# Kernel optimization log

Measured on AMD Instinct MI355X. Metric: run time of the kernel, lower is better.

Reference implementation:

```python
import jax, jax.numpy as jnp
import numpy as np

N0, N1, N2 = 100000, 300000, 150000
P = 2
DIM = 64


def spmm(rows, cols, vals, dense, n_rows):
    # sparse[n_rows, n_cols] @ dense[n_cols, d] via gather + segment_sum
    return jax.ops.segment_sum(vals[:, None] * dense[cols], rows, num_segments=n_rows)


def powcat(X, p):
    # torch.cat([X**1, ..., X**p], dim=1)
    return jnp.concatenate([X ** n for n in range(1, p + 1)], axis=1)


def setup_inputs() -> dict:
    key = jax.random.key(0)
    ks = iter(jax.random.split(key, 64))

    def randn(shape, scale=1.0):
        return jax.random.normal(next(ks), shape, dtype=jnp.float32) * scale

    def sparse(nr, nc, nnz):
        r = jax.random.randint(next(ks), (nnz,), 0, nr, dtype=jnp.int32)
        c = jax.random.randint(next(ks), (nnz,), 0, nc, dtype=jnp.int32)
        v = randn((nnz,), 0.1)
        return r, c, v

    inp = {}
    inp["X0"] = randn((N0, DIM))
    inp["X1"] = randn((N1, DIM))
    inp["X2"] = randn((N2, DIM))
    for name, nr, nc, nnz in [
        ("L0", N0, N0, 1000000),
        ("L1", N1, N1, 2400000),
        ("L2", N2, N2, 1200000),
        ("D1invB1", N0, N1, 600000),
        ("D2B1TD1inv", N1, N0, 600000),
        ("B2TD2inv", N2, N1, 450000),
        ("B2D3", N1, N2, 450000),
    ]:
        r, c, v = sparse(nr, nc, nnz)
        inp[name + "_rows"], inp[name + "_cols"], inp[name + "_vals"] = r, c, v
    wscale = 1.0 / np.sqrt(DIM * P)
    for name in ["n2n", "n2e", "e2e", "e2n", "e2t", "t2e", "t2t"]:
        inp["W_" + name] = randn((DIM * P, DIM), wscale)
        inp["b_" + name] = randn((DIM,), wscale)
    return inp


def reference(X0, X1, X2,
              L0_rows, L0_cols, L0_vals,
              L1_rows, L1_cols, L1_vals,
              L2_rows, L2_cols, L2_vals,
              D1invB1_rows, D1invB1_cols, D1invB1_vals,
              D2B1TD1inv_rows, D2B1TD1inv_cols, D2B1TD1inv_vals,
              B2TD2inv_rows, B2TD2inv_cols, B2TD2inv_vals,
              B2D3_rows, B2D3_cols, B2D3_vals,
              W_n2n, b_n2n, W_n2e, b_n2e, W_e2e, b_e2e, W_e2n, b_e2n,
              W_e2t, b_e2t, W_t2e, b_t2e, W_t2t, b_t2t):
    X0c = powcat(X0, P)  # [N0, 2*d]
    X1c = powcat(X1, P)  # [N1, 2*d]
    X2c = powcat(X2, P)  # [N2, 2*d]

    n2n = spmm(L0_rows, L0_cols, L0_vals, X0c @ W_n2n + b_n2n, N0)
    n2e = spmm(D2B1TD1inv_rows, D2B1TD1inv_cols, D2B1TD1inv_vals, X0c @ W_n2e + b_n2e, N1)
    e2n = spmm(D1invB1_rows, D1invB1_cols, D1invB1_vals, X1c @ W_e2n + b_e2n, N0)
    e2e = spmm(L1_rows, L1_cols, L1_vals, X1c @ W_e2e + b_e2e, N1)
    e2t = spmm(B2TD2inv_rows, B2TD2inv_cols, B2TD2inv_vals, X1c @ W_e2t + b_e2t, N2)
    t2t = spmm(L2_rows, L2_cols, L2_vals, X2c @ W_t2t + b_t2t, N2)
    t2e = spmm(B2D3_rows, B2D3_cols, B2D3_vals, X2c @ W_t2e + b_t2e, N1)

    Y0 = 0.5 * jax.nn.relu(n2n + e2n)
    Y1 = (1.0 / 3.0) * jax.nn.relu(e2e + n2e + t2e)
    Y2 = 0.5 * jax.nn.relu(t2t + e2t)
    return (Y0, Y1, Y2)
```

## Files before the change

### kernel.cpp

```cpp
#include <hip/hip_runtime.h>
#include <hip/hip_bf16.h>


#define RPB 128
#define COL_MASK 0x7FFFFu
#define LROW_SH 19
#define DID_SH 26
#define MAXNB 4352
#define MAXNG 544
#define GRID_BIN 256
#define SPMM_GRID 2048

#define SORT_PH     16384
#define SORT_LOG    14
#define SORT_MAXBIN 2048
#define SORT_CAP    (SORT_PH + SORT_MAXBIN)
#define MAXPH 8

typedef __attribute__((ext_vector_type(8))) short short8;
typedef __attribute__((ext_vector_type(4))) float f32x4;

__device__ __forceinline__ int   ntld_i(const int* p)   { return __builtin_nontemporal_load(p); }
__device__ __forceinline__ float ntld_f(const float* p) { return __builtin_nontemporal_load(p); }
__device__ __forceinline__ float4 ntld_f4(const float* p) {
    const unsigned long long* q = (const unsigned long long*)p;
    unsigned long long a = __builtin_nontemporal_load(q);
    unsigned long long b = __builtin_nontemporal_load(q + 1);
    float4 v;
    v.x = __uint_as_float((unsigned)a);
    v.y = __uint_as_float((unsigned)(a >> 32));
    v.z = __uint_as_float((unsigned)b);
    v.w = __uint_as_float((unsigned)(b >> 32));
    return v;
}
__device__ __forceinline__ void ntst_f4(float* p, float4 v) {
    unsigned long long a = (unsigned long long)__float_as_uint(v.x)
                         | ((unsigned long long)__float_as_uint(v.y) << 32);
    unsigned long long b = (unsigned long long)__float_as_uint(v.z)
                         | ((unsigned long long)__float_as_uint(v.w) << 32);
    unsigned long long* q = (unsigned long long*)p;
    __builtin_nontemporal_store(a, q);
    __builtin_nontemporal_store(b, q + 1);
}

__device__ __forceinline__ unsigned short f2bf(float f) {
    unsigned u = __float_as_uint(f);
    unsigned r = u + 0x7FFFu + ((u >> 16) & 1u);
    return (unsigned short)(r >> 16);
}

__device__ __forceinline__ void split8(float4 a0, float4 a1, short8& hi, short8& lo) {
    float v[8] = {a0.x, a0.y, a0.z, a0.w, a1.x, a1.y, a1.z, a1.w};
    #pragma unroll
    for (int e = 0; e < 8; ++e) {
        unsigned short h = f2bf(v[e]);
        float hf = __uint_as_float((unsigned)h << 16);
        hi[e] = (short)h;
        lo[e] = (short)f2bf(v[e] - hf);
    }
}

struct WAll { const float* w[7]; };

__global__ __launch_bounds__(256) void winit(WAll wa, unsigned short* __restrict__ frags)
{
    const int s = blockIdx.x;
    const float* __restrict__ W = wa.w[s];
    unsigned short* __restrict__ out = frags + (size_t)s * 16384;
    for (int slot = threadIdx.x; slot < 1024; slot += 256) {
        const int l  = slot & 63;
        const int nf = (slot >> 6) & 3;
        const int kk = slot >> 8;
        const int col = nf * 16 + (l & 15);
        const int kb  = kk * 32 + 8 * (l >> 4);
        short8 vh, vl;
        #pragma unroll
        for (int e = 0; e < 8; ++e) {
            float w = W[(size_t)(kb + e) * 64 + col];
            unsigned short h = f2bf(w);
            float hf = __uint_as_float((unsigned)h << 16);
            vh[e] = (short)h;
            vl[e] = (short)f2bf(w - hf);
        }
        *(short8*)(out + ((size_t)((kk * 4 + nf) * 2 + 0) * 64 + l) * 8) = vh;
        *(short8*)(out + ((size_t)((kk * 4 + nf) * 2 + 1) * 64 + l) * 8) = vl;
    }
}

__device__ __forceinline__ void mfma_set(
    const short8 Ah[4], const short8 Al[4],
    const unsigned short* __restrict__ F, const float* __restrict__ bias,
    unsigned short* __restrict__ D, int nrows, int row0w, int l)
{
    const int lg = l >> 4, lr = l & 15;
    const short8* __restrict__ Fv = (const short8*)F;
    f32x4 acc[4];
    #pragma unroll
    for (int nf = 0; nf < 4; ++nf) {
        float b = bias[nf * 16 + lr];
        f32x4 bi = {b, b, b, b};
        acc[nf] = bi;
    }
    #pragma unroll
    for (int kk = 0; kk < 4; ++kk) {
        #pragma unroll
        for (int nf = 0; nf < 4; ++nf) {
            short8 bh = Fv[((kk * 4 + nf) * 2 + 0) * 64 + l];
            short8 bl = Fv[((kk * 4 + nf) * 2 + 1) * 64 + l];
            acc[nf] = __builtin_amdgcn_mfma_f32_16x16x32_bf16(Ah[kk], bh, acc[nf], 0, 0, 0);
            acc[nf] = __builtin_amdgcn_mfma_f32_16x16x32_bf16(Al[kk], bh, acc[nf], 0, 0, 0);
            acc[nf] = __builtin_amdgcn_mfma_f32_16x16x32_bf16(Ah[kk], bl, acc[nf], 0, 0, 0);
        }
    }
    #pragma unroll
    for (int nf = 0; nf < 4; ++nf) {
        #pragma unroll
        for (int j = 0; j < 4; ++j) {
            int row = row0w + lg * 4 + j;
            if (row < nrows)
                D[(size_t)row * 64 + nf * 16 + lr] = f2bf(acc[nf][j]);
        }
    }
}

__global__ __launch_bounds__(256) void gemm_powcat_mfma(
    const float* __restrict__ X, int nrows, int nsets,
    const unsigned short* __restrict__ F0, const float* __restrict__ b0, unsigned short* __restrict__ D0,
    const unsigned short* __restrict__ F1, const float* __restrict__ b1, unsigned short* __restrict__ D1,
    const unsigned short* __restrict__ F2, const float* __restrict__ b2, unsigned short* __restrict__ D2)
{
    __shared__ float Xs[64][68];
    const int tid = threadIdx.x;
    const int row0 = blockIdx.x * 64;

    #pragma unroll
    for (int it = 0; it < 4; ++it) {
        int idx = tid + it * 256;
        int r = idx >> 4, c4 = idx & 15;
        float4 v = make_float4(0.f, 0.f, 0.f, 0.f);
        if (row0 + r < nrows)
            v = ntld_f4(X + (size_t)(row0 + r) * 64 + c4 * 4);
        *(float4*)&Xs[r][c4 * 4] = v;
    }
    __syncthreads();

    const int w = tid >> 6, l = tid & 63;
    const int lg = l >> 4, lr = l & 15;

    short8 Ah[4], Al[4];
    #pragma unroll
    for (int kk = 0; kk < 4; ++kk) {
        const float* p = &Xs[w * 16 + lr][(kk & 1) * 32 + 8 * lg];
        float4 a0 = *(const float4*)p;
        float4 a1 = *(const float4*)(p + 4);
        if (kk >= 2) {
            a0.x *= a0.x; a0.y *= a0.y; a0.z *= a0.z; a0.w *= a0.w;
            a1.x *= a1.x; a1.y *= a1.y; a1.z *= a1.z; a1.w *= a1.w;
        }
        split8(a0, a1, Ah[kk], Al[kk]);
    }

    const int row0w = row0 + w * 16;
    mfma_set(Ah, Al, F0, b0, D0, nrows, row0w, l);
    if (nsets > 1) mfma_set(Ah, Al, F1, b1, D1, nrows, row0w, l);
    if (nsets > 2) mfma_set(Ah, Al, F2, b2, D2, nrows, row0w, l);
}

struct Bin7 {
    const int *r0, *r1, *r2, *r3, *r4, *r5, *r6;
    const int *c0, *c1, *c2, *c3, *c4, *c5, *c6;
    const float *v0, *v1, *v2, *v3, *v4, *v5, *v6;
    int p1, p2, p3, p4, p5, p6, p7;
    int t0, t1, t2, t3, t4, t5, t6;
};

struct Ent { int r; int tb; unsigned cw; float v; };

template<bool FULL>
__device__ __forceinline__ Ent decode(const Bin7& B, int i) {
    Ent e;
    if (i < B.p1) {
        int li = i;
        e.r = ntld_i(B.r0 + li); e.tb = B.t0;
        if (FULL) { e.cw = (unsigned)ntld_i(B.c0 + li) | (0u << DID_SH); e.v = ntld_f(B.v0 + li); }
    } else if (i < B.p2) {
        int li = i - B.p1;
        e.r = ntld_i(B.r1 + li); e.tb = B.t1;
        if (FULL) { e.cw = (unsigned)ntld_i(B.c1 + li) | (1u << DID_SH); e.v = ntld_f(B.v1 + li); }
    } else if (i < B.p3) {
        int li = i - B.p2;
        e.r = ntld_i(B.r2 + li); e.tb = B.t2;
        if (FULL) { e.cw = (unsigned)ntld_i(B.c2 + li) | (2u << DID_SH); e.v = ntld_f(B.v2 + li); }
    } else if (i < B.p4) {
        int li = i - B.p3;
        e.r = ntld_i(B.r3 + li); e.tb = B.t3;
        if (FULL) { e.cw = (unsigned)ntld_i(B.c3 + li) | (3u << DID_SH); e.v = ntld_f(B.v3 + li); }
    } else if (i < B.p5) {
        int li = i - B.p4;
        e.r = ntld_i(B.r4 + li); e.tb = B.t4;
        if (FULL) { e.cw = (unsigned)ntld_i(B.c4 + li) | (4u << DID_SH); e.v = ntld_f(B.v4 + li); }
    } else if (i < B.p6) {
        int li = i - B.p5;
        e.r = ntld_i(B.r5 + li); e.tb = B.t5;
        if (FULL) { e.cw = (unsigned)ntld_i(B.c5 + li) | (5u << DID_SH); e.v = ntld_f(B.v5 + li); }
    } else {
        int li = i - B.p6;
        e.r = ntld_i(B.r6 + li); e.tb = B.t6;
        if (FULL) { e.cw = (unsigned)ntld_i(B.c6 + li) | (6u << DID_SH); e.v = ntld_f(B.v6 + li); }
    }
    return e;
}

__global__ __launch_bounds__(1024) void bhist_grp(
    Bin7 B, int* __restrict__ gcount, int NG, int chunk)
{
    __shared__ int h[MAXNG];
    for (int i = threadIdx.x; i < NG; i += 1024) h[i] = 0;
    __syncthreads();
    const int s = blockIdx.x * chunk;
    int e = s + chunk;  if (e > B.p7) e = B.p7;
    for (int i = s + threadIdx.x; i < e; i += 1024) {
        Ent en = decode<false>(B, i);
        atomicAdd(&h[(en.tb + (en.r >> 7)) >> 3], 1);
    }
    __syncthreads();
    for (int i = threadIdx.x; i < NG; i += 1024)
        if (h[i]) atomicAdd(&gcount[i], h[i]);
}

__global__ __launch_bounds__(1024) void scatter_grp(
    Bin7 B, int* __restrict__ gcur, uint2* __restrict__ payA,
    int NG, int chunk)
{
    __shared__ int lbase[MAXNG];
    __shared__ int lcur[MAXNG];
    for (int i = threadIdx.x; i < NG; i += 1024) lcur[i] = 0;
    __syncthreads();
    const int s = blockIdx.x * chunk;
    int e = s + chunk;  if (e > B.p7) e = B.p7;

    for (int i = s + threadIdx.x; i < e; i += 1024) {
        Ent en = decode<false>(B, i);
        atomicAdd(&lcur[(en.tb + (en.r >> 7)) >> 3], 1);
    }
    __syncthreads();
    for (int i = threadIdx.x; i < NG; i += 1024) {
        int c = lcur[i];
        lbase[i] = c ? atomicAdd(&gcur[i], c) : 0;
        lcur[i] = 0;
    }
    __syncthreads();
    for (int i = s + threadIdx.x; i < e; i += 1024) {
        Ent en = decode<true>(B, i);
        int b = en.tb + (en.r >> 7);
        int g = b >> 3;
        int pos = lbase[g] + atomicAdd(&lcur[g], 1);
        unsigned col = en.cw & COL_MASK;
        unsigned did = en.cw >> DID_SH;
        unsigned cwA = col | ((unsigned)(en.r & 127) << LROW_SH)
                     | ((unsigned)(b & 7) << 26) | (did << 29);
        payA[pos] = make_uint2(cwA, __float_as_uint(en.v));
    }
}

__global__ __launch_bounds__(1024) void sort_grp(
    const uint2* __restrict__ payA, const int* __restrict__ goff,
    const int* __restrict__ gcur, int* __restrict__ rowoff,
    int* __restrict__ bend, uint2* __restrict__ payB, int NBtot)
{
    __shared__ uint2 lpay[SORT_CAP];
    __shared__ int cnt[1024];
    __shared__ int off[1024];
    __shared__ int wsum[16];
    __shared__ int phstart[MAXPH + 1];
    __shared__ int s_nph, s_maxbin;

    const int g = blockIdx.x;
    const int tid = threadIdx.x;
    const int seg0 = goff[g], seg1 = gcur[g];
    const int n = seg1 - seg0;

    cnt[tid] = 0;
    if (tid == 0) s_maxbin = 0;
    __syncthreads();
    for (int i = seg0 + tid; i < seg1; i += 1024) {
        unsigned w = __builtin_nontemporal_load(&payA[i].x);
        atomicAdd(&cnt[(w >> 19) & 1023], 1);
    }
    __syncthreads();

    const int lane = tid & 63, wv = tid >> 6;
    const int tot = cnt[tid];
    atomicMax(&s_maxbin, tot);
    int x = tot;
    #pragma unroll
    for (int o = 1; o < 64; o <<= 1) {
        int y = __shfl_up(x, o);
        if (lane >= o) x += y;
    }
    if (lane == 63) wsum[wv] = x;
    __syncthreads();
    if (tid < 16) {
        int ss = wsum[tid];
        #pragma unroll
        for (int o = 1; o < 16; o <<= 1) {
            int y = __shfl_up(ss, o, 16);
            if (tid >= o) ss += y;
        }
        wsum[tid] = ss;
    }
    __syncthreads();
    const int excl = (x - tot) + ((wv == 0) ? 0 : wsum[wv - 1]);
    off[tid] = excl;
    rowoff[(size_t)g * 1024 + tid] = seg0 + excl;
    {
        int b = g * 8 + (tid >> 7);
        if (b < NBtot && (tid & 127) == 127) bend[b] = seg0 + excl + tot;
    }
    __syncthreads();
    cnt[tid] = excl;
    {
        int p = excl >> SORT_LOG;
        int pprev = (tid == 0) ? -1 : (off[tid - 1] >> SORT_LOG);
        for (int q = pprev + 1; q <= p && q <= MAXPH; ++q) phstart[q] = excl;
        if (tid == 1023) s_nph = p + 1;
    }
    __syncthreads();

    const int nph = s_nph;
    if (n <= 0) return;

    if (s_maxbin <= SORT_MAXBIN && nph <= MAXPH) {
        for (int ph = 0; ph < nph; ++ph) {
            const int ps = phstart[ph];
            const int pe = (ph + 1 < nph) ? phstart[ph + 1] : n;
            for (int i = seg0 + tid; i < seg1; i += 1024) {
                unsigned long long pv = __builtin_nontemporal_load(
                    (const unsigned long long*)(payA + i));
                unsigned w = (unsigned)pv;
                int bin = (w >> 19) & 1023;
                if ((off[bin] >> SORT_LOG) == ph) {
                    int pos = atomicAdd(&cnt[bin], 1);
                    lpay[pos - ps] = make_uint2(w, (unsigned)(pv >> 32));
                }
            }
            __syncthreads();
            for (int k = tid; k < pe - ps; k += 1024) {
                uint2 pv = lpay[k];
                unsigned cw = (pv.x & 0x03FFFFFFu) | ((pv.x >> 29) << 26);
                unsigned long long o2 = (unsigned long long)cw
                                      | ((unsigned long long)pv.y << 32);
                __builtin_nontemporal_store(o2,
                    (unsigned long long*)(payB + seg0 + ps + k));
            }
            __syncthreads();
        }
    } else {
        for (int i = seg0 + tid; i < seg1; i += 1024) {
            unsigned long long pv = __builtin_nontemporal_load(
                (const unsigned long long*)(payA + i));
            unsigned w = (unsigned)pv;
            int bin = (w >> 19) & 1023;
            int pos = seg0 + atomicAdd(&cnt[bin], 1);
            unsigned cw = (w & 0x03FFFFFFu) | ((w >> 29) << 26);
            payB[pos] = make_uint2(cw, (unsigned)(pv >> 32));
        }
    }
}

__global__ __launch_bounds__(1024) void scan_small(
    const int* __restrict__ in, int* __restrict__ boff,
    int* __restrict__ bcur, int n)
{
    __shared__ int wsum[16];
    __shared__ int carry;
    const int tid = threadIdx.x, lane = tid & 63, wv = tid >> 6;
    if (tid == 0) carry = 0;
    __syncthreads();
    for (int base = 0; base < n; base += 4096) {
        int i = base + tid * 4;
        int v0 = (i + 0 < n) ? in[i + 0] : 0;
        int v1 = (i + 1 < n) ? in[i + 1] : 0;
        int v2 = (i + 2 < n) ? in[i + 2] : 0;
        int v3 = (i + 3 < n) ? in[i + 3] : 0;
        int tsum = v0 + v1 + v2 + v3;
        int x = tsum;
        #pragma unroll
        for (int off = 1; off < 64; off <<= 1) {
            int y = __shfl_up(x, off);
            if (lane >= off) x += y;
        }
        if (lane == 63) wsum[wv] = x;
        int c0 = carry;
        __syncthreads();
        if (tid < 16) {
            int ss = wsum[tid];
            #pragma unroll
            for (int off = 1; off < 16; off <<= 1) {
                int y = __shfl_up(ss, off, 16);
                if (tid >= off) ss += y;
            }
            wsum[tid] = ss;
        }
        __syncthreads();
        int wpre = (wv == 0) ? 0 : wsum[wv - 1];
        int excl = c0 + wpre + (x - tsum);
        if (i + 0 < n) { boff[i + 0] = excl; bcur[i + 0] = excl; } excl += v0;
        if (i + 1 < n) { boff[i + 1] = excl; bcur[i + 1] = excl; } excl += v1;
        if (i + 2 < n) { boff[i + 2] = excl; bcur[i + 2] = excl; } excl += v2;
        if (i + 3 < n) { boff[i + 3] = excl; bcur[i + 3] = excl; }
        __syncthreads();
        if (tid == 0) carry = c0 + wsum[15];
        __syncthreads();
    }
}

__device__ __forceinline__ float mval(uint2 p, int didMask) {
    int did = (int)(p.x >> DID_SH) & 7;
    return ((didMask >> did) & 1) ? __uint_as_float(p.y) : 0.f;
}
__device__ __forceinline__ uint2 dgather(uint2 p, int l,
    const unsigned short* const* dptr)
{
    const uint2* Dg = reinterpret_cast<const uint2*>(dptr[(p.x >> DID_SH) & 7]);
    return Dg[(size_t)(p.x & COL_MASK) * 16 + l];
}
__device__ __forceinline__ void facc(float4& a, float v, uint2 d) {
    a.x = fmaf(v, __uint_as_float((d.x & 0xFFFFu) << 16), a.x);
    a.y = fmaf(v, __uint_as_float(d.x & 0xFFFF0000u), a.y);
    a.z = fmaf(v, __uint_as_float((d.y & 0xFFFFu) << 16), a.z);
    a.w = fmaf(v, __uint_as_float(d.y & 0xFFFF0000u), a.w);
}

__device__ __forceinline__ float4 row_accum(
    const uint2* __restrict__ payB, int js, int je,
    const unsigned short* const* dptr, int l, int didMask)
{
    float4 a = make_float4(0.f, 0.f, 0.f, 0.f);
    const int n = je - js;
    if (n <= 0) return a;
    const uint2* base = payB + js;
    uint2 p0 = base[0];
    uint2 p1 = base[(n > 1) ? 1 : 0];
    float v0 = mval(p0, didMask);
    float v1 = (n > 1) ? mval(p1, didMask) : 0.f;
    uint2 d0 = dgather(p0, l, dptr);
    uint2 d1 = dgather(p1, l, dptr);
    int i = 0;
    while (true) {
        int i2 = (i + 2 < n) ? i + 2 : n - 1;
        int i3 = (i + 3 < n) ? i + 3 : n - 1;
        uint2 q0 = base[i2];
        uint2 q1 = base[i3];
        float w0 = (i + 2 < n) ? mval(q0, didMask) : 0.f;
        float w1 = (i + 3 < n) ? mval(q1, didMask) : 0.f;
        uint2 e0 = dgather(q0, l, dptr);
        uint2 e1 = dgather(q1, l, dptr);
        facc(a, v0, d0);
        facc(a, v1, d1);
        i += 2;
        if (i >= n) break;
        v0 = w0; v1 = w1; d0 = e0; d1 = e1;
    }
    return a;
}

__global__ __launch_bounds__(256) void spmm_stream_all(
    const uint2* __restrict__ payB, const int* __restrict__ rowoff,
    const int* __restrict__ bend,
    const unsigned short* __restrict__ d0, const unsigned short* __restrict__ d1,
    const unsigned short* __restrict__ d2, const unsigned short* __restrict__ d3,
    const unsigned short* __restrict__ d4, const unsigned short* __restrict__ d5,
    const unsigned short* __restrict__ d6,
    float* __restrict__ out, int NB0, int NB01, int NBall,
    int N0, int N1, int N2)
{
    __shared__ const unsigned short* dptr[8];
    const int tid = threadIdx.x;
    if (tid < 8) {
        const unsigned short* tbl[8] = {d0, d1, d2, d3, d4, d5, d6, d0};
        dptr[tid] = tbl[tid];
    }
    __syncthreads();

    const int qw = tid >> 4, l = tid & 15;

    for (int t = blockIdx.x; t < NBall; t += gridDim.x) {
        int tb, nrows; float scale; float* oseg;
        if (t < NB0)       { tb = 0;    nrows = N0; oseg = out;                          scale = 0.5f; }
        else if (t < NB01) { tb = NB0;  nrows = N1; oseg = out + (size_t)N0 * 64;        scale = 1.0f / 3.0f; }
        else               { tb = NB01; nrows = N2; oseg = out + (size_t)(N0 + N1) * 64; scale = 0.5f; }
        const int row0 = (t - tb) * RPB;
        const int rbase = t * RPB;
        const int bendt = bend[t];

        #pragma unroll 1
        for (int rr = 0; rr < 8; ++rr) {
            const int lr = rr * 16 + qw;
            const int row = row0 + lr;
            const int js = rowoff[rbase + lr];
            const int je = (lr == 127) ? bendt : rowoff[rbase + lr + 1];
            float4 a = row_accum(payB, js, je, dptr, l, 0x7F);
            if (row < nrows) {
                float* o = oseg + (size_t)row * 64 + l * 4;
                a.x = fmaxf(a.x, 0.f) * scale;
                a.y = fmaxf(a.y, 0.f) * scale;
                a.z = fmaxf(a.z, 0.f) * scale;
                a.w = fmaxf(a.w, 0.f) * scale;
                ntst_f4(o, a);
            }
        }
    }
}

__global__ __launch_bounds__(256) void spmm_stream7(
    const uint2* __restrict__ payB, const int* __restrict__ rowoff,
    const int* __restrict__ bend,
    const unsigned short* __restrict__ d0, const unsigned short* __restrict__ d1,
    const unsigned short* __restrict__ d2, const unsigned short* __restrict__ d3,
    const unsigned short* __restrict__ d4, const unsigned short* __restrict__ d5,
    const unsigned short* __restrict__ d6,
    float* __restrict__ out, int tile0, int nrows,
    int firstWrite, int doRelu, float scale, int didMask)
{
    __shared__ const unsigned short* dptr[8];
    const int tid = threadIdx.x;
    if (tid < 8) {
        const unsigned short* tbl[8] = {d0, d1, d2, d3, d4, d5, d6, d0};
        dptr[tid] = tbl[tid];
    }
    __syncthreads();

    const int t = tile0 + blockIdx.x;
    const int qw = tid >> 4, l = tid & 15;
    const int row0 = blockIdx.x * RPB;
    const int rbase = t * RPB;
    const int bendt = bend[t];

    #pragma unroll 1
    for (int rr = 0; rr < 8; ++rr) {
        const int lr = rr * 16 + qw;
        const int row = row0 + lr;
        const int js = rowoff[rbase + lr];
        const int je = (lr == 127) ? bendt : rowoff[rbase + lr + 1];
        float4 a = row_accum(payB, js, je, dptr, l, didMask);

        if (row < nrows) {
            float* o = out + (size_t)row * 64 + l * 4;
            if (!firstWrite) {
                float4 cur = *reinterpret_cast<float4*>(o);
                a.x += cur.x; a.y += cur.y; a.z += cur.z; a.w += cur.w;
            }
            if (doRelu) {
                a.x = fmaxf(a.x, 0.f) * scale;
                a.y = fmaxf(a.y, 0.f) * scale;
                a.z = fmaxf(a.z, 0.f) * scale;
                a.w = fmaxf(a.w, 0.f) * scale;
            }
            ntst_f4(o, a);
        }
    }
}

extern "C" void kernel_launch(void* const* d_in, const int* in_sizes, int n_in,
                              void* d_out, int out_size, void* d_ws, size_t ws_size,
                              hipStream_t stream)
{
    const float* X0 = (const float*)d_in[0];
    const float* X1 = (const float*)d_in[1];
    const float* X2 = (const float*)d_in[2];
    const int N0 = in_sizes[0] / 64;
    const int N1 = in_sizes[1] / 64;
    const int N2 = in_sizes[2] / 64;

    auto Wp = [&](int i) { return (const float*)d_in[24 + 2 * i]; };
    auto bp = [&](int i) { return (const float*)d_in[25 + 2 * i]; };
    auto Sr = [&](int i) { return (const int*)d_in[3 + 3 * i]; };
    auto Sc = [&](int i) { return (const int*)d_in[4 + 3 * i]; };
    auto Sv = [&](int i) { return (const float*)d_in[5 + 3 * i]; };
    auto Sn = [&](int i) { return in_sizes[3 + 3 * i]; };

    const size_t offY1 = (size_t)N0 * 64;
    const size_t offY2 = (size_t)(N0 + N1) * 64;
    const float TH = 1.0f / 3.0f;

    const int NB0 = (N0 + RPB - 1) / RPB;
    const int NB1 = (N1 + RPB - 1) / RPB;
    const int NB2 = (N2 + RPB - 1) / RPB;

    float* out = (float*)d_out;
    auto align256 = [](size_t x) { return (x + 255) & ~(size_t)255; };

    const size_t FRAG_SET = 16384;
    const size_t fragB = align256(7 * FRAG_SET * sizeof(unsigned short));
    if (ws_size <= fragB) return;
    unsigned short* wfrags = (unsigned short*)d_ws;
    char* ws = (char*)d_ws + fragB;
    const size_t ws_avail = ws_size - fragB;
    auto wf = [&](int i) { return wfrags + (size_t)i * FRAG_SET; };

    WAll wa;
    for (int i = 0; i < 7; ++i) wa.w[i] = Wp(i);
    winit<<<7, 256, 0, stream>>>(wa, wfrags);

    const int NBall = NB0 + NB1 + NB2;
    const int NGall = (NBall + 7) / 8;
    const int nnzAll = Sn(0)+Sn(1)+Sn(2)+Sn(3)+Sn(4)+Sn(5)+Sn(6);
    const size_t payT1 = align256((size_t)nnzAll * sizeof(uint2));
    const size_t cntT1 = align256((size_t)(NBall + 8) * sizeof(int));
    const size_t rowT1 = align256((size_t)NGall * 1024 * sizeof(int));
    const size_t denseT1 = ((size_t)2*N0 + 3*N1 + 2*N2) * 64 * sizeof(unsigned short);
    const size_t regionT1 = denseT1 > payT1 ? denseT1 : payT1;
    const size_t needT1 = payT1 + 4 * cntT1 + rowT1 + regionT1;

    if (ws_avail >= needT1 && NBall <= MAXNB) {
        uint2* payB  = (uint2*)ws;
        int* goff    = (int*)(ws + payT1);
        int* gcur    = (int*)(ws + payT1 + 1 * cntT1);
        int* bend    = (int*)(ws + payT1 + 2 * cntT1);
        int* gcount  = (int*)(ws + payT1 + 3 * cntT1);
        int* rowoff  = (int*)(ws + payT1 + 4 * cntT1);
        char* region = ws + payT1 + 4 * cntT1 + rowT1;
        uint2* payA  = (uint2*)region;
        unsigned short* db = (unsigned short*)region;
        unsigned short* dn2n = db;
        unsigned short* de2n = dn2n + (size_t)N0 * 64;
        unsigned short* dn2e = de2n + (size_t)N1 * 64;
        unsigned short* de2e = dn2e + (size_t)N0 * 64;
        unsigned short* dt2e = de2e + (size_t)N1 * 64;
        unsigned short* de2t = dt2e + (size_t)N2 * 64;
        unsigned short* dt2t = de2t + (size_t)N1 * 64;

        Bin7 B;
        B.r0 = Sr(0); B.c0 = Sc(0); B.v0 = Sv(0);
        B.r1 = Sr(3); B.c1 = Sc(3); B.v1 = Sv(3);
        B.r2 = Sr(4); B.c2 = Sc(4); B.v2 = Sv(4);
        B.r3 = Sr(1); B.c3 = Sc(1); B.v3 = Sv(1);
        B.r4 = Sr(6); B.c4 = Sc(6); B.v4 = Sv(6);
        B.r5 = Sr(5); B.c5 = Sc(5); B.v5 = Sv(5);
        B.r6 = Sr(2); B.c6 = Sc(2); B.v6 = Sv(2);
        B.p1 = Sn(0);
        B.p2 = B.p1 + Sn(3);
        B.p3 = B.p2 + Sn(4);
        B.p4 = B.p3 + Sn(1);
        B.p5 = B.p4 + Sn(6);
        B.p6 = B.p5 + Sn(5);
        B.p7 = B.p6 + Sn(2);
        B.t0 = 0;   B.t1 = 0;
        B.t2 = NB0; B.t3 = NB0; B.t4 = NB0;
        B.t5 = NB0 + NB1; B.t6 = NB0 + NB1;

        const int chunk = (B.p7 + GRID_BIN - 1) / GRID_BIN;
        hipMemsetAsync(gcount, 0, (size_t)NGall * sizeof(int), stream);
        bhist_grp<<<GRID_BIN, 1024, 0, stream>>>(B, gcount, NGall, chunk);
        scan_small<<<1, 1024, 0, stream>>>(gcount, goff, gcur, NGall);
        scatter_grp<<<GRID_BIN, 1024, 0, stream>>>(B, gcur, payA, NGall, chunk);
        sort_grp<<<NGall, 1024, 0, stream>>>(payA, goff, gcur, rowoff, bend, payB, NBall);

        gemm_powcat_mfma<<<(N0 + 63) / 64, 256, 0, stream>>>(
            X0, N0, 2,
            wf(0), bp(0), dn2n,
            wf(1), bp(1), dn2e,
            wf(0), bp(0), dn2n);
        gemm_powcat_mfma<<<(N1 + 63) / 64, 256, 0, stream>>>(
            X1, N1, 3,
            wf(3), bp(3), de2n,
            wf(2), bp(2), de2e,
            wf(4), bp(4), de2t);
        gemm_powcat_mfma<<<(N2 + 63) / 64, 256, 0, stream>>>(
            X2, N2, 2,
            wf(5), bp(5), dt2e,
            wf(6), bp(6), dt2t,
            wf(5), bp(5), dt2e);

        const int grid = NBall < SPMM_GRID ? NBall : SPMM_GRID;
        spmm_stream_all<<<grid, 256, 0, stream>>>(payB, rowoff, bend,
            dn2n, de2n, dn2e, de2e, dt2e, de2t, dt2t,
            out, NB0, NB0 + NB1, NBall, N0, N1, N2);
        return;
    }

    const int NBtotA = NB0 + NB2;
    const int NBmax = NBtotA > NB1 ? NBtotA : NB1;
    const int NGmax = (NBmax + 7) / 8;
    const int nnzA = Sn(0) + Sn(3) + Sn(5) + Sn(2);
    const int nnzB = Sn(4) + Sn(6) + Sn(1);
    const int nnzMax = nnzA > nnzB ? nnzA : nnzB;

    const size_t payBsz = align256((size_t)nnzMax * sizeof(uint2));
    const size_t cntB = align256((size_t)(NBmax + 8) * sizeof(int));
    const size_t rowB = align256((size_t)NGmax * 1024 * sizeof(int));
    const size_t denseOff = payBsz + 4 * cntB + rowB;

    uint2* bpayB = (uint2*)ws;
    int* goff    = (int*)(ws + payBsz);
    int* gcur    = (int*)(ws + payBsz + 1 * cntB);
    int* bend    = (int*)(ws + payBsz + 2 * cntB);
    int* gcount  = (int*)(ws + payBsz + 3 * cntB);
    int* rowoff  = (int*)(ws + payBsz + 4 * cntB);
    unsigned short* dense = (unsigned short*)(ws + denseOff);
    uint2* payA  = (uint2*)dense;

    const size_t need_full = denseOff +
        ((size_t)N0 + N2 + N1) * 64 * sizeof(unsigned short);
    const bool fullB = (ws_avail >= need_full);

    {
        Bin7 B;
        B.r0 = Sr(0); B.c0 = Sc(0); B.v0 = Sv(0);
        B.r1 = Sr(3); B.c1 = Sc(3); B.v1 = Sv(3);
        B.r2 = Sr(5); B.c2 = Sc(5); B.v2 = Sv(5);
        B.r3 = Sr(2); B.c3 = Sc(2); B.v3 = Sv(2);
        B.r4 = B.r3; B.c4 = B.c3; B.v4 = B.v3;
        B.r5 = B.r3; B.c5 = B.c3; B.v5 = B.v3;
        B.r6 = B.r3; B.c6 = B.c3; B.v6 = B.v3;
        B.p1 = Sn(0);
        B.p2 = B.p1 + Sn(3);
        B.p3 = B.p2 + Sn(5);
        B.p4 = B.p3 + Sn(2);
        B.p5 = B.p4; B.p6 = B.p4; B.p7 = B.p4;
        B.t0 = 0; B.t1 = 0; B.t2 = NB0; B.t3 = NB0;
        B.t4 = NB0; B.t5 = NB0; B.t6 = NB0;

        const int NGA = (NBtotA + 7) / 8;
        const int chunk = (B.p7 + GRID_BIN - 1) / GRID_BIN;
        hipMemsetAsync(gcount, 0, (size_t)NGA * sizeof(int), stream);
        bhist_grp<<<GRID_BIN, 1024, 0, stream>>>(B, gcount, NGA, chunk);
        scan_small<<<1, 1024, 0, stream>>>(gcount, goff, gcur, NGA);
        scatter_grp<<<GRID_BIN, 1024, 0, stream>>>(B, gcur, payA, NGA, chunk);
        sort_grp<<<NGA, 1024, 0, stream>>>(payA, goff, gcur, rowoff, bend, bpayB, NBtotA);

        unsigned short* dn2n = dense;
        unsigned short* de2n = dense + (size_t)N0 * 64;
        gemm_powcat_mfma<<<(N0 + 63) / 64, 256, 0, stream>>>(
            X0, N0, 1, wf(0), bp(0), dn2n,
            wf(0), bp(0), dn2n, wf(0), bp(0), dn2n);
        gemm_powcat_mfma<<<(N1 + 63) / 64, 256, 0, stream>>>(
            X1, N1, 1, wf(3), bp(3), de2n,
            wf(3), bp(3), de2n, wf(3), bp(3), de2n);
        spmm_stream7<<<NB0, 256, 0, stream>>>(bpayB, rowoff, bend,
            dn2n, de2n, dn2n, dn2n, dn2n, dn2n, dn2n,
            out, 0, N0, 1, 1, 0.5f, 0x7F);

        unsigned short* de2t = dense;
        unsigned short* dt2t = dense + (size_t)N1 * 64;
        gemm_powcat_mfma<<<(N1 + 63) / 64, 256, 0, stream>>>(
            X1, N1, 1, wf(4), bp(4), de2t,
            wf(4), bp(4), de2t, wf(4), bp(4), de2t);
        gemm_powcat_mfma<<<(N2 + 63) / 64, 256, 0, stream>>>(
            X2, N2, 1, wf(6), bp(6), dt2t,
            wf(6), bp(6), dt2t, wf(6), bp(6), dt2t);
        spmm_stream7<<<NB2, 256, 0, stream>>>(bpayB, rowoff, bend,
            de2t, de2t, de2t, dt2t, de2t, de2t, de2t,
            out + offY2, NB0, N2, 1, 1, 0.5f, 0x7F);
    }

    {
        Bin7 B;
        B.r0 = Sr(4); B.c0 = Sc(4); B.v0 = Sv(4);
        B.r1 = Sr(6); B.c1 = Sc(6); B.v1 = Sv(6);
        B.r2 = Sr(1); B.c2 = Sc(1); B.v2 = Sv(1);
        B.r3 = B.r2; B.c3 = B.c2; B.v3 = B.v2;
        B.r4 = B.r2; B.c4 = B.c2; B.v4 = B.v2;
        B.r5 = B.r2; B.c5 = B.c2; B.v5 = B.v2;
        B.r6 = B.r2; B.c6 = B.c2; B.v6 = B.v2;
        B.p1 = Sn(4);
        B.p2 = B.p1 + Sn(6);
        B.p3 = B.p2 + Sn(1);
        B.p4 = B.p3; B.p5 = B.p3; B.p6 = B.p3; B.p7 = B.p3;
        B.t0 = 0; B.t1 = 0; B.t2 = 0; B.t3 = 0; B.t4 = 0; B.t5 = 0; B.t6 = 0;

        const int NGB = (NB1 + 7) / 8;
        const int chunk = (B.p7 + GRID_BIN - 1) / GRID_BIN;
        hipMemsetAsync(gcount, 0, (size_t)NGB * sizeof(int), stream);
        bhist_grp<<<GRID_BIN, 1024, 0, stream>>>(B, gcount, NGB, chunk);
        scan_small<<<1, 1024, 0, stream>>>(gcount, goff, gcur, NGB);
        scatter_grp<<<GRID_BIN, 1024, 0, stream>>>(B, gcur, payA, NGB, chunk);
        sort_grp<<<NGB, 1024, 0, stream>>>(payA, goff, gcur, rowoff, bend, bpayB, NB1);

        if (fullB) {
            unsigned short* dn2e = dense;
            unsigned short* dt2e = dense + (size_t)N0 * 64;
            unsigned short* de2e = dense + ((size_t)N0 + N2) * 64;
            gemm_powcat_mfma<<<(N0 + 63) / 64, 256, 0, stream>>>(
                X0, N0, 1, wf(1), bp(1), dn2e,
                wf(1), bp(1), dn2e, wf(1), bp(1), dn2e);
            gemm_powcat_mfma<<<(N2 + 63) / 64, 256, 0, stream>>>(
                X2, N2, 1, wf(5), bp(5), dt2e,
                wf(5), bp(5), dt2e, wf(5), bp(5), dt2e);
            gemm_powcat_mfma<<<(N1 + 63) / 64, 256, 0, stream>>>(
                X1, N1, 1, wf(2), bp(2), de2e,
                wf(2), bp(2), de2e, wf(2), bp(2), de2e);
            spmm_stream7<<<NB1, 256, 0, stream>>>(bpayB, rowoff, bend,
                dn2e, dt2e, de2e, dn2e, dn2e, dn2e, dn2e,
                out + offY1, 0, N1, 1, 1, TH, 0x7F);
        } else {
            unsigned short* dn2e = dense;
            unsigned short* dt2e = dense + (size_t)N0 * 64;
            gemm_powcat_mfma<<<(N0 + 63) / 64, 256, 0, stream>>>(
                X0, N0, 1, wf(1), bp(1), dn2e,
                wf(1), bp(1), dn2e, wf(1), bp(1), dn2e);
            gemm_powcat_mfma<<<(N2 + 63) / 64, 256, 0, stream>>>(
                X2, N2, 1, wf(5), bp(5), dt2e,
                wf(5), bp(5), dt2e, wf(5), bp(5), dt2e);
            spmm_stream7<<<NB1, 256, 0, stream>>>(bpayB, rowoff, bend,
                dn2e, dt2e, dn2e, dn2e, dn2e, dn2e, dn2e,
                out + offY1, 0, N1, 1, 0, 0.f, 0x3);
            unsigned short* de2e = dense;
            gemm_powcat_mfma<<<(N1 + 63) / 64, 256, 0, stream>>>(
                X1, N1, 1, wf(2), bp(2), de2e,
                wf(2), bp(2), de2e, wf(2), bp(2), de2e);
            spmm_stream7<<<NB1, 256, 0, stream>>>(bpayB, rowoff, bend,
                de2e, de2e, de2e, de2e, de2e, de2e, de2e,
                out + offY1, 0, N1, 0, 1, TH, 0x4);
        }
    }
}
```

Before: 517.3 us.

## Deepen SpMM gather prefetch to four and use atomic work queue for row blocks

The row accumulation loop now keeps four payload entries and their dense-row gathers in flight instead of two, and reads payloads with nontemporal loads. Row blocks are now claimed dynamically through a global atomic counter, reset by a memset before launch, instead of a fixed grid-stride assignment, to balance uneven block costs. This adds register pressure, two block barriers per tile and one extra memset launch.

```diff
diff --git a/kernel.cpp b/kernel.cpp
--- a/kernel.cpp
+++ b/kernel.cpp
@@ -22,6 +22,10 @@
 
 __device__ __forceinline__ int   ntld_i(const int* p)   { return __builtin_nontemporal_load(p); }
 __device__ __forceinline__ float ntld_f(const float* p) { return __builtin_nontemporal_load(p); }
+__device__ __forceinline__ uint2 ntld_u2(const uint2* p) {
+    unsigned long long v = __builtin_nontemporal_load((const unsigned long long*)p);
+    return make_uint2((unsigned)v, (unsigned)(v >> 32));
+}
 __device__ __forceinline__ float4 ntld_f4(const float* p) {
     const unsigned long long* q = (const unsigned long long*)p;
     unsigned long long a = __builtin_nontemporal_load(q);
@@ -440,27 +444,52 @@
     const int n = je - js;
     if (n <= 0) return a;
     const uint2* base = payB + js;
-    uint2 p0 = base[0];
-    uint2 p1 = base[(n > 1) ? 1 : 0];
+    const int jlast = n - 1;
+
+    uint2 p0 = ntld_u2(base);
+    uint2 p1 = ntld_u2(base + (1 < jlast ? 1 : jlast));
+    uint2 p2 = ntld_u2(base + (2 < jlast ? 2 : jlast));
+    uint2 p3 = ntld_u2(base + (3 < jlast ? 3 : jlast));
     float v0 = mval(p0, didMask);
-    float v1 = (n > 1) ? mval(p1, didMask) : 0.f;
+    float v1 = (1 < n) ? mval(p1, didMask) : 0.f;
+    float v2 = (2 < n) ? mval(p2, didMask) : 0.f;
+    float v3 = (3 < n) ? mval(p3, didMask) : 0.f;
     uint2 d0 = dgather(p0, l, dptr);
     uint2 d1 = dgather(p1, l, dptr);
+    uint2 d2 = dgather(p2, l, dptr);
+    uint2 d3 = dgather(p3, l, dptr);
+
     int i = 0;
-    while (true) {
-        int i2 = (i + 2 < n) ? i + 2 : n - 1;
-        int i3 = (i + 3 < n) ? i + 3 : n - 1;
-        uint2 q0 = base[i2];
-        uint2 q1 = base[i3];
-        float w0 = (i + 2 < n) ? mval(q0, didMask) : 0.f;
-        float w1 = (i + 3 < n) ? mval(q1, didMask) : 0.f;
-        uint2 e0 = dgather(q0, l, dptr);
-        uint2 e1 = dgather(q1, l, dptr);
+    for (;;) {
+        const bool more = (i + 4 < n);
+        float w0, w1, w2, w3;
+        uint2 e0, e1, e2, e3;
+        if (more) {
+            int i4 = i + 4;
+            int i5 = (i + 5 < jlast) ? i + 5 : jlast;
+            int i6 = (i + 6 < jlast) ? i + 6 : jlast;
+            int i7 = (i + 7 < jlast) ? i + 7 : jlast;
+            uint2 q0 = ntld_u2(base + i4);
+            uint2 q1 = ntld_u2(base + i5);
+            uint2 q2 = ntld_u2(base + i6);
+            uint2 q3 = ntld_u2(base + i7);
+            w0 = mval(q0, didMask);
+            w1 = (i + 5 < n) ? mval(q1, didMask) : 0.f;
+            w2 = (i + 6 < n) ? mval(q2, didMask) : 0.f;
+            w3 = (i + 7 < n) ? mval(q3, didMask) : 0.f;
+            e0 = dgather(q0, l, dptr);
+            e1 = dgather(q1, l, dptr);
+            e2 = dgather(q2, l, dptr);
+            e3 = dgather(q3, l, dptr);
+        }
         facc(a, v0, d0);
         facc(a, v1, d1);
-        i += 2;
-        if (i >= n) break;
-        v0 = w0; v1 = w1; d0 = e0; d1 = e1;
+        facc(a, v2, d2);
+        facc(a, v3, d3);
+        if (!more) break;
+        i += 4;
+        v0 = w0; v1 = w1; v2 = w2; v3 = w3;
+        d0 = e0; d1 = e1; d2 = e2; d3 = e3;
     }
     return a;
 }
@@ -473,19 +502,25 @@
     const unsigned short* __restrict__ d4, const unsigned short* __restrict__ d5,
     const unsigned short* __restrict__ d6,
     float* __restrict__ out, int NB0, int NB01, int NBall,
-    int N0, int N1, int N2)
+    int N0, int N1, int N2, int* __restrict__ wq)
 {
     __shared__ const unsigned short* dptr[8];
+    __shared__ int s_t;
     const int tid = threadIdx.x;
     if (tid < 8) {
         const unsigned short* tbl[8] = {d0, d1, d2, d3, d4, d5, d6, d0};
         dptr[tid] = tbl[tid];
     }
-    __syncthreads();
 
     const int qw = tid >> 4, l = tid & 15;
 
-    for (int t = blockIdx.x; t < NBall; t += gridDim.x) {
+    for (;;) {
+        __syncthreads();
+        if (tid == 0) s_t = atomicAdd(wq, 1);
+        __syncthreads();
+        const int t = s_t;
+        if (t >= NBall) break;
+
         int tb, nrows; float scale; float* oseg;
         if (t < NB0)       { tb = 0;    nrows = N0; oseg = out;                          scale = 0.5f; }
         else if (t < NB01) { tb = NB0;  nrows = N1; oseg = out + (size_t)N0 * 64;        scale = 1.0f / 3.0f; }
@@ -673,10 +708,12 @@
             wf(6), bp(6), dt2t,
             wf(5), bp(5), dt2e);
 
+        int* wq = gcount;
+        hipMemsetAsync(wq, 0, sizeof(int), stream);
         const int grid = NBall < SPMM_GRID ? NBall : SPMM_GRID;
         spmm_stream_all<<<grid, 256, 0, stream>>>(payB, rowoff, bend,
             dn2n, de2n, dn2e, de2e, dt2e, de2t, dt2t,
-            out, NB0, NB0 + NB1, NBall, N0, N1, N2);
+            out, NB0, NB0 + NB1, NBall, N0, N1, N2, wq);
         return;
     }
 
```

New measurement: 577.2 us. 1.12x slower.

## Use per-block histogram scan to drop scatter recount and global atomics

Applied to the files above, without the earlier changes.

The bucketing pipeline now writes a per-block, per-group histogram matrix and scans it with the existing single-block scan. This gives each scatter block its own base offset directly, so scatter2 skips the second counting pass over the input and the global atomic base reservation. The sort kernel reads its segment bounds from the scanned matrix. The row accumulation loop is also rewritten to handle one entry per iteration with a two-deep prefetch instead of the unrolled pair. The cost is a much larger scan (NG*256 entries) done by one block, which could become a serial bottleneck.

```diff
diff --git a/kernel.cpp b/kernel.cpp
--- a/kernel.cpp
+++ b/kernel.cpp
@@ -211,8 +211,8 @@
     return e;
 }
 
-__global__ __launch_bounds__(1024) void bhist_grp(
-    Bin7 B, int* __restrict__ gcount, int NG, int chunk)
+__global__ __launch_bounds__(1024) void bhist_wr(
+    Bin7 B, int* __restrict__ ghist, int NG, int chunk)
 {
     __shared__ int h[MAXNG];
     for (int i = threadIdx.x; i < NG; i += 1024) h[i] = 0;
@@ -225,31 +225,22 @@
     }
     __syncthreads();
     for (int i = threadIdx.x; i < NG; i += 1024)
-        if (h[i]) atomicAdd(&gcount[i], h[i]);
-}
-
-__global__ __launch_bounds__(1024) void scatter_grp(
-    Bin7 B, int* __restrict__ gcur, uint2* __restrict__ payA,
+        ghist[(size_t)i * GRID_BIN + blockIdx.x] = h[i];
+}
+
+__global__ __launch_bounds__(1024) void scatter2(
+    Bin7 B, const int* __restrict__ gbase, uint2* __restrict__ payA,
     int NG, int chunk)
 {
     __shared__ int lbase[MAXNG];
     __shared__ int lcur[MAXNG];
-    for (int i = threadIdx.x; i < NG; i += 1024) lcur[i] = 0;
+    for (int i = threadIdx.x; i < NG; i += 1024) {
+        lbase[i] = gbase[(size_t)i * GRID_BIN + blockIdx.x];
+        lcur[i] = 0;
+    }
     __syncthreads();
     const int s = blockIdx.x * chunk;
     int e = s + chunk;  if (e > B.p7) e = B.p7;
-
-    for (int i = s + threadIdx.x; i < e; i += 1024) {
-        Ent en = decode<false>(B, i);
-        atomicAdd(&lcur[(en.tb + (en.r >> 7)) >> 3], 1);
-    }
-    __syncthreads();
-    for (int i = threadIdx.x; i < NG; i += 1024) {
-        int c = lcur[i];
-        lbase[i] = c ? atomicAdd(&gcur[i], c) : 0;
-        lcur[i] = 0;
-    }
-    __syncthreads();
     for (int i = s + threadIdx.x; i < e; i += 1024) {
         Ent en = decode<true>(B, i);
         int b = en.tb + (en.r >> 7);
@@ -264,9 +255,9 @@
 }
 
 __global__ __launch_bounds__(1024) void sort_grp(
-    const uint2* __restrict__ payA, const int* __restrict__ goff,
-    const int* __restrict__ gcur, int* __restrict__ rowoff,
-    int* __restrict__ bend, uint2* __restrict__ payB, int NBtot)
+    const uint2* __restrict__ payA, const int* __restrict__ gbase,
+    int* __restrict__ rowoff, int* __restrict__ bend,
+    uint2* __restrict__ payB, int NBtot)
 {
     __shared__ uint2 lpay[SORT_CAP];
     __shared__ int cnt[1024];
@@ -277,7 +268,8 @@
 
     const int g = blockIdx.x;
     const int tid = threadIdx.x;
-    const int seg0 = goff[g], seg1 = gcur[g];
+    const int seg0 = gbase[(size_t)g * GRID_BIN];
+    const int seg1 = gbase[(size_t)(g + 1) * GRID_BIN];
     const int n = seg1 - seg0;
 
     cnt[tid] = 0;
@@ -437,30 +429,24 @@
     const unsigned short* const* dptr, int l, int didMask)
 {
     float4 a = make_float4(0.f, 0.f, 0.f, 0.f);
-    const int n = je - js;
-    if (n <= 0) return a;
-    const uint2* base = payB + js;
-    uint2 p0 = base[0];
-    uint2 p1 = base[(n > 1) ? 1 : 0];
-    float v0 = mval(p0, didMask);
-    float v1 = (n > 1) ? mval(p1, didMask) : 0.f;
-    uint2 d0 = dgather(p0, l, dptr);
-    uint2 d1 = dgather(p1, l, dptr);
-    int i = 0;
-    while (true) {
-        int i2 = (i + 2 < n) ? i + 2 : n - 1;
-        int i3 = (i + 3 < n) ? i + 3 : n - 1;
-        uint2 q0 = base[i2];
-        uint2 q1 = base[i3];
-        float w0 = (i + 2 < n) ? mval(q0, didMask) : 0.f;
-        float w1 = (i + 3 < n) ? mval(q1, didMask) : 0.f;
-        uint2 e0 = dgather(q0, l, dptr);
-        uint2 e1 = dgather(q1, l, dptr);
-        facc(a, v0, d0);
-        facc(a, v1, d1);
-        i += 2;
-        if (i >= n) break;
-        v0 = w0; v1 = w1; d0 = e0; d1 = e1;
+    if (js >= je) return a;
+    const int jlast = je - 1;
+    uint2 pA = payB[js];
+    uint2 pB = payB[js < jlast ? js + 1 : jlast];
+    const uint2* DgA = reinterpret_cast<const uint2*>(dptr[(pA.x >> DID_SH) & 7]);
+    uint2 dA = DgA[(size_t)(pA.x & COL_MASK) * 16 + l];
+    float vA = ((didMask >> ((pA.x >> DID_SH) & 7)) & 1) ? __uint_as_float(pA.y) : 0.f;
+
+    for (int j = js; j < je; ++j) {
+        uint2 dcur = dA;
+        float vcur = vA;
+        uint2 pN = pB;
+        int j2 = j + 2 <= jlast ? j + 2 : jlast;
+        pB = payB[j2];
+        const uint2* Dg = reinterpret_cast<const uint2*>(dptr[(pN.x >> DID_SH) & 7]);
+        dA = Dg[(size_t)(pN.x & COL_MASK) * 16 + l];
+        vA = ((didMask >> ((pN.x >> DID_SH) & 7)) & 1) ? __uint_as_float(pN.y) : 0.f;
+        facc(a, vcur, dcur);
     }
     return a;
 }
@@ -609,18 +595,18 @@
     const size_t payT1 = align256((size_t)nnzAll * sizeof(uint2));
     const size_t cntT1 = align256((size_t)(NBall + 8) * sizeof(int));
     const size_t rowT1 = align256((size_t)NGall * 1024 * sizeof(int));
+    const size_t gszT1 = align256(((size_t)NGall * GRID_BIN + 1) * sizeof(int));
     const size_t denseT1 = ((size_t)2*N0 + 3*N1 + 2*N2) * 64 * sizeof(unsigned short);
     const size_t regionT1 = denseT1 > payT1 ? denseT1 : payT1;
-    const size_t needT1 = payT1 + 4 * cntT1 + rowT1 + regionT1;
+    const size_t needT1 = payT1 + cntT1 + rowT1 + 2 * gszT1 + regionT1;
 
     if (ws_avail >= needT1 && NBall <= MAXNB) {
         uint2* payB  = (uint2*)ws;
-        int* goff    = (int*)(ws + payT1);
-        int* gcur    = (int*)(ws + payT1 + 1 * cntT1);
-        int* bend    = (int*)(ws + payT1 + 2 * cntT1);
-        int* gcount  = (int*)(ws + payT1 + 3 * cntT1);
-        int* rowoff  = (int*)(ws + payT1 + 4 * cntT1);
-        char* region = ws + payT1 + 4 * cntT1 + rowT1;
+        int* bend    = (int*)(ws + payT1);
+        int* rowoff  = (int*)(ws + payT1 + cntT1);
+        int* ghist   = (int*)(ws + payT1 + cntT1 + rowT1);
+        int* gbase   = (int*)(ws + payT1 + cntT1 + rowT1 + gszT1);
+        char* region = ws + payT1 + cntT1 + rowT1 + 2 * gszT1;
         uint2* payA  = (uint2*)region;
         unsigned short* db = (unsigned short*)region;
         unsigned short* dn2n = db;
@@ -651,11 +637,12 @@
         B.t5 = NB0 + NB1; B.t6 = NB0 + NB1;
 
         const int chunk = (B.p7 + GRID_BIN - 1) / GRID_BIN;
-        hipMemsetAsync(gcount, 0, (size_t)NGall * sizeof(int), stream);
-        bhist_grp<<<GRID_BIN, 1024, 0, stream>>>(B, gcount, NGall, chunk);
-        scan_small<<<1, 1024, 0, stream>>>(gcount, goff, gcur, NGall);
-        scatter_grp<<<GRID_BIN, 1024, 0, stream>>>(B, gcur, payA, NGall, chunk);
-        sort_grp<<<NGall, 1024, 0, stream>>>(payA, goff, gcur, rowoff, bend, payB, NBall);
+        const int nscan = NGall * GRID_BIN + 1;
+        hipMemsetAsync(ghist + (nscan - 1), 0, sizeof(int), stream);
+        bhist_wr<<<GRID_BIN, 1024, 0, stream>>>(B, ghist, NGall, chunk);
+        scan_small<<<1, 1024, 0, stream>>>(ghist, gbase, gbase, nscan);
+        scatter2<<<GRID_BIN, 1024, 0, stream>>>(B, gbase, payA, NGall, chunk);
+        sort_grp<<<NGall, 1024, 0, stream>>>(payA, gbase, rowoff, bend, payB, NBall);
 
         gemm_powcat_mfma<<<(N0 + 63) / 64, 256, 0, stream>>>(
             X0, N0, 2,
@@ -690,14 +677,14 @@
     const size_t payBsz = align256((size_t)nnzMax * sizeof(uint2));
     const size_t cntB = align256((size_t)(NBmax + 8) * sizeof(int));
     const size_t rowB = align256((size_t)NGmax * 1024 * sizeof(int));
-    const size_t denseOff = payBsz + 4 * cntB + rowB;
+    const size_t gszB = align256(((size_t)NGmax * GRID_BIN + 1) * sizeof(int));
+    const size_t denseOff = payBsz + cntB + rowB + 2 * gszB;
 
     uint2* bpayB = (uint2*)ws;
-    int* goff    = (int*)(ws + payBsz);
-    int* gcur    = (int*)(ws + payBsz + 1 * cntB);
-    int* bend    = (int*)(ws + payBsz + 2 * cntB);
-    int* gcount  = (int*)(ws + payBsz + 3 * cntB);
-    int* rowoff  = (int*)(ws + payBsz + 4 * cntB);
+    int* bend    = (int*)(ws + payBsz);
+    int* rowoff  = (int*)(ws + payBsz + cntB);
+    int* ghist   = (int*)(ws + payBsz + cntB + rowB);
+    int* gbase   = (int*)(ws + payBsz + cntB + rowB + gszB);
     unsigned short* dense = (unsigned short*)(ws + denseOff);
     uint2* payA  = (uint2*)dense;
 
@@ -724,11 +711,12 @@
 
         const int NGA = (NBtotA + 7) / 8;
         const int chunk = (B.p7 + GRID_BIN - 1) / GRID_BIN;
-        hipMemsetAsync(gcount, 0, (size_t)NGA * sizeof(int), stream);
-        bhist_grp<<<GRID_BIN, 1024, 0, stream>>>(B, gcount, NGA, chunk);
-        scan_small<<<1, 1024, 0, stream>>>(gcount, goff, gcur, NGA);
-        scatter_grp<<<GRID_BIN, 1024, 0, stream>>>(B, gcur, payA, NGA, chunk);
-        sort_grp<<<NGA, 1024, 0, stream>>>(payA, goff, gcur, rowoff, bend, bpayB, NBtotA);
+        const int nscan = NGA * GRID_BIN + 1;
+        hipMemsetAsync(ghist + (nscan - 1), 0, sizeof(int), stream);
+        bhist_wr<<<GRID_BIN, 1024, 0, stream>>>(B, ghist, NGA, chunk);
+        scan_small<<<1, 1024, 0, stream>>>(ghist, gbase, gbase, nscan);
+        scatter2<<<GRID_BIN, 1024, 0, stream>>>(B, gbase, payA, NGA, chunk);
+        sort_grp<<<NGA, 1024, 0, stream>>>(payA, gbase, rowoff, bend, bpayB, NBtotA);
 
         unsigned short* dn2n = dense;
         unsigned short* de2n = dense + (size_t)N0 * 64;
@@ -772,11 +760,12 @@
 
         const int NGB = (NB1 + 7) / 8;
         const int chunk = (B.p7 + GRID_BIN - 1) / GRID_BIN;
-        hipMemsetAsync(gcount, 0, (size_t)NGB * sizeof(int), stream);
-        bhist_grp<<<GRID_BIN, 1024, 0, stream>>>(B, gcount, NGB, chunk);
-        scan_small<<<1, 1024, 0, stream>>>(gcount, goff, gcur, NGB);
-        scatter_grp<<<GRID_BIN, 1024, 0, stream>>>(B, gcur, payA, NGB, chunk);
-        sort_grp<<<NGB, 1024, 0, stream>>>(payA, goff, gcur, rowoff, bend, bpayB, NB1);
+        const int nscan = NGB * GRID_BIN + 1;
+        hipMemsetAsync(ghist + (nscan - 1), 0, sizeof(int), stream);
+        bhist_wr<<<GRID_BIN, 1024, 0, stream>>>(B, ghist, NGB, chunk);
+        scan_small<<<1, 1024, 0, stream>>>(ghist, gbase, gbase, nscan);
+        scatter2<<<GRID_BIN, 1024, 0, stream>>>(B, gbase, payA, NGB, chunk);
+        sort_grp<<<NGB, 1024, 0, stream>>>(payA, gbase, rowoff, bend, bpayB, NB1);
 
         if (fullB) {
             unsigned short* dn2e = dense;
```

Measured after the change: 646.9 us. 1.25x slower.
